# Optimization experiments

Measured on AMD Instinct MI355X. Metric: run time of the kernel, lower is better.

Reference implementation:

```python
import jax, jax.numpy as jnp
import numpy as np

N = 50000      # nodes
E = 600000     # edges
F_IN = 128     # input features
H = 128        # hidden
C = 40         # classes


def _glorot(key, shape):
    lim = float(np.sqrt(6.0 / (shape[0] + shape[1])))
    return jax.random.uniform(key, shape, jnp.float32, -lim, lim)


def setup_inputs() -> dict:
    key = jax.random.key(0)
    ks = jax.random.split(key, 16)
    inp = {
        "x": jax.random.normal(ks[0], (N, F_IN), jnp.float32),
        "edge_index": jax.random.randint(ks[1], (2, E), 0, N, jnp.int64),
    }
    # SAGEConv params: Wl (neighbor branch, with bias), Wr (root branch), stored [in, out]
    dims = [(F_IN, H), (H, H), (H, H)]
    for i, (din, dout) in enumerate(dims, start=1):
        inp[f"Wl{i}"] = _glorot(ks[2 * i], (din, dout))
        inp[f"bl{i}"] = jnp.zeros((dout,), jnp.float32)
        inp[f"Wr{i}"] = _glorot(ks[2 * i + 1], (din, dout))
    inp["W_lin1"] = _glorot(ks[10], (H, H))
    inp["b_lin1"] = jnp.zeros((H,), jnp.float32)
    inp["W_lin2"] = _glorot(ks[11], (H, C))
    inp["b_lin2"] = jnp.zeros((C,), jnp.float32)
    return inp


def _sage_conv(x, src, dst, Wl, bl, Wr):
    # mean-aggregate neighbor features at destination nodes
    msgs = x[src]  # [E, d] gather
    agg = jax.ops.segment_sum(msgs, dst, num_segments=N)
    deg = jax.ops.segment_sum(jnp.ones((E,), x.dtype), dst, num_segments=N)
    agg = agg / jnp.clip(deg, 1.0)[:, None]
    return agg @ Wl + bl + x @ Wr


def reference(x, edge_index, Wl1, bl1, Wr1, Wl2, bl2, Wr2, Wl3, bl3, Wr3,
              W_lin1, b_lin1, W_lin2, b_lin2):
    src, dst = edge_index[0], edge_index[1]
    h = jax.nn.relu(_sage_conv(x, src, dst, Wl1, bl1, Wr1))
    h = jax.nn.relu(_sage_conv(h, src, dst, Wl2, bl2, Wr2))
    h = jax.nn.relu(_sage_conv(h, src, dst, Wl3, bl3, Wr3))
    h = jax.nn.relu(h @ W_lin1 + b_lin1)
    # dropout: inference mode (training=False) -> identity
    logits = h @ W_lin2 + b_lin2
    return jax.nn.log_softmax(logits, axis=-1)
```

## Files before the change

kernel.cpp:

```cpp
#include <hip/hip_runtime.h>
#include <hip/hip_bf16.h>
#include <math.h>

#define NNODES 50000
#define NEDGES 600000
#define FDIM   128
#define NCLS   40
#define SLOTS  64
#define CVT_BLOCKS 6250
#define PACK_BLOCKS 62
#define CZ_BLOCKS 196
#define PREP_TOTAL (CVT_BLOCKS + PACK_BLOCKS + CZ_BLOCKS)
#define NT16 (NNODES / 16)

typedef __hip_bfloat16 bf16;
typedef short bf16x8 __attribute__((ext_vector_type(8)));
typedef short bf16x4 __attribute__((ext_vector_type(4)));
typedef float f32x4  __attribute__((ext_vector_type(4)));

__device__ __forceinline__ float b2f(short u) {
    union { unsigned int i; float f; } cv;
    cv.i = ((unsigned int)(unsigned short)u) << 16;
    return cv.f;
}
__device__ __forceinline__ short f2b(float f) {
    bf16 h = __float2bfloat16(f);
    return *(const short*)&h;
}
__device__ __forceinline__ float ldf(const void* p, int fp32, int idx) {
    return fp32 ? ((const float*)p)[idx]
                : __bfloat162float(((const bf16*)p)[idx]);
}
__device__ __forceinline__ int wave_is_fp32(const unsigned* p, int lane) {
    unsigned w = p[lane];
    unsigned e = (w >> 7) & 0xFFu;
    int inr = (e >= 100u && e <= 140u) ? 1 : 0;
    return (int)__popcll(__ballot(inr)) < 32;
}
__device__ __forceinline__ int lidx(int row, int col) {
    return row * 128 + ((((col >> 3) ^ (row & 15)) << 3) | (col & 7));
}

__global__ void k_prep(const void* __restrict__ xin,
                       const void* Wl1, const void* Wr1, const void* Wl2,
                       const void* Wr2, const void* Wl3, const void* Wr3,
                       const void* Wlin1, const void* Wlin2,
                       const void* b1, const void* b2, const void* b3,
                       const void* b4, const void* b5,
                       int* __restrict__ cursor, bf16* __restrict__ xb,
                       bf16x8* __restrict__ packed, float* __restrict__ biasf) {
    int b = blockIdx.x, tid = threadIdx.x, lane = tid & 63;
    if (b < CVT_BLOCKS) {
        int xf = wave_is_fp32((const unsigned*)xin, lane);
        int i = b * 256 + tid;
        if (xf) {
            float4 v = ((const float4*)xin)[i];
            bf16x4 o;
            o[0] = f2b(v.x); o[1] = f2b(v.y); o[2] = f2b(v.z); o[3] = f2b(v.w);
            ((bf16x4*)xb)[i] = o;
        } else {
            ((uint2*)xb)[i] = ((const uint2*)xin)[i];
        }
        return;
    }
    if (b >= CVT_BLOCKS + PACK_BLOCKS) {
        int i = (b - CVT_BLOCKS - PACK_BLOCKS) * 256 + tid;
        if (i < NNODES) cursor[i] = 0;
        return;
    }
    int wf = wave_is_fp32((const unsigned*)Wl1, lane);
    int lb = b - CVT_BLOCKS;
    if (lb >= 59) {
        int t = (lb - 59) * 256 + tid;
        if (t >= 5 * 128) return;
        int which = t >> 7, idx = t & 127;
        const void* srcs[5] = {b1, b2, b3, b4, b5};
        int n = (which == 4) ? NCLS : 128;
        float v = 0.f;
        if (idx < n) v = ldf(srcs[which], wf, idx);
        biasf[t] = v;
        return;
    }
    int t2 = lb * 256 + tid;
    int frag = t2 >> 6;
    if (frag >= 236) return;
    int q = lane >> 4, l16 = lane & 15;
    const void* W;
    int kbase, n, ldw = 128, nvalid = 128;
    if (frag < 192) {
        int g = frag >> 6, local = frag & 63;
        int kt = local >> 3, nt = local & 7;
        const void* Wl = (g == 0) ? Wl1 : (g == 1) ? Wl2 : Wl3;
        const void* Wr = (g == 0) ? Wr1 : (g == 1) ? Wr2 : Wr3;
        W = (kt < 4) ? Wl : Wr;
        kbase = (kt & 3) * 32;
        n = nt * 16 + l16;
    } else if (frag < 224) {
        int local = frag - 192;
        int kt = local >> 3, nt = local & 7;
        W = Wlin1; kbase = kt * 32; n = nt * 16 + l16;
    } else {
        int local = frag - 224;
        int kt = local / 3, nt = local % 3;
        W = Wlin2; kbase = kt * 32; n = nt * 16 + l16;
        ldw = NCLS; nvalid = NCLS;
    }
    bf16x8 v;
#pragma unroll
    for (int j = 0; j < 8; j++) {
        float e = 0.f;
        if (n < nvalid) e = ldf(W, wf, (kbase + q * 8 + j) * ldw + n);
        v[j] = f2b(e);
    }
    packed[frag * 64 + lane] = v;
}

__global__ void k_fill(const int* __restrict__ e32, const long long* __restrict__ e64,
                       int* __restrict__ cursor, int* __restrict__ edge_src) {
    int lane = threadIdx.x & 63;
    unsigned hw = ((const unsigned*)e32)[2 * lane + 1];
    int is64 = (__ballot(hw != 0u) == 0ull) ? 1 : 0;
    int i = blockIdx.x * 256 + threadIdx.x;
    if (i >= NEDGES) return;
    int srcn = is64 ? (int)e64[i] : e32[i];
    int dstn = is64 ? (int)e64[NEDGES + i] : e32[NEDGES + i];
    int pos = atomicAdd(&cursor[dstn], 1);
    if (pos < SLOTS) edge_src[dstn * SLOTS + pos] = srcn;
}

__device__ __forceinline__ void agg_wave(const bf16* __restrict__ x,
        const int* __restrict__ deg, const int* __restrict__ edge_src,
        short* __restrict__ lds, int rowbase, int wave, int lane) {
    const int g = lane >> 4, c = lane & 15;
    const int base = rowbase + wave * 8;
    int dgv = deg[base];
    int eidx = edge_src[base * SLOTS + lane];
    if ((unsigned)eidx >= NNODES) eidx = 0;
#pragma unroll
    for (int t = 0; t < 8; t++) {
        int dgn = 0;
        if (t < 7) dgn = deg[base + t + 1];
        int dcap = dgv < SLOTS ? ((dgv + 15) & ~15) : SLOTS;
        float acc[8];
#pragma unroll
        for (int e = 0; e < 8; e++) acc[e] = 0.f;
        for (int i = 0; i < dcap; i += 16) {
            float m0 = (i + g < dgv) ? 1.f : 0.f;
            float m1 = (i + 4 + g < dgv) ? 1.f : 0.f;
            float m2 = (i + 8 + g < dgv) ? 1.f : 0.f;
            float m3 = (i + 12 + g < dgv) ? 1.f : 0.f;
            unsigned o0 = (unsigned)(__shfl(eidx, i + g)      * FDIM + c * 8);
            unsigned o1 = (unsigned)(__shfl(eidx, i + 4 + g)  * FDIM + c * 8);
            unsigned o2 = (unsigned)(__shfl(eidx, i + 8 + g)  * FDIM + c * 8);
            unsigned o3 = (unsigned)(__shfl(eidx, i + 12 + g) * FDIM + c * 8);
            bf16x8 v0 = *(const bf16x8*)(x + o0);
            bf16x8 v1 = *(const bf16x8*)(x + o1);
            bf16x8 v2 = *(const bf16x8*)(x + o2);
            bf16x8 v3 = *(const bf16x8*)(x + o3);
#pragma unroll
            for (int e = 0; e < 8; e++) {
                acc[e] = fmaf(b2f(v0[e]), m0, acc[e]);
                acc[e] = fmaf(b2f(v1[e]), m1, acc[e]);
                acc[e] = fmaf(b2f(v2[e]), m2, acc[e]);
                acc[e] = fmaf(b2f(v3[e]), m3, acc[e]);
            }
        }
        int en = 0;
        if (t < 7) {
            en = edge_src[(base + t + 1) * SLOTS + lane];
            if ((unsigned)en >= NNODES) en = 0;
        }
#pragma unroll
        for (int e = 0; e < 8; e++) {
            float a = acc[e];
            a += __shfl_xor(a, 16);
            a += __shfl_xor(a, 32);
            acc[e] = a;
        }
        if (g == 0) {
            float inv = (dgv > 0) ? 1.f / (float)dgv : 0.f;
            bf16x8 o;
#pragma unroll
            for (int e = 0; e < 8; e++) o[e] = f2b(acc[e] * inv);
            *(bf16x8*)(lds + lidx(wave * 8 + t, c * 8)) = o;
        }
        dgv = dgn; eidx = en;
    }
}

template <bool TO_LDS>
__device__ __forceinline__ void gemm_phase(int rowbase, int lane, int wave,
        short* __restrict__ aggL, const bf16* __restrict__ xroot,
        const bf16x8* __restrict__ packed, const float* __restrict__ bias,
        bf16* __restrict__ out) {
    const int q = lane >> 4, l16 = lane & 15;
    const unsigned rowA = (unsigned)(rowbase + l16);
    f32x4 acc[4];
#pragma unroll
    for (int n = 0; n < 4; n++) acc[n] = (f32x4){0.f, 0.f, 0.f, 0.f};
#pragma unroll 2
    for (int kt = 0; kt < 8; kt++) {
        bf16x8 a;
        if (kt < 4)
            a = *(const bf16x8*)(aggL + lidx(l16, kt * 32 + q * 8));
        else
            a = *(const bf16x8*)(xroot + rowA * FDIM + (kt - 4) * 32 + q * 8);
        bf16x8 b[4];
#pragma unroll
        for (int n = 0; n < 4; n++)
            b[n] = packed[(kt * 8 + wave * 4 + n) * 64 + lane];
#pragma unroll
        for (int n = 0; n < 4; n++)
            acc[n] = __builtin_amdgcn_mfma_f32_16x16x32_bf16(a, b[n], acc[n], 0, 0, 0);
    }
    if (TO_LDS) __syncthreads();
#pragma unroll
    for (int n = 0; n < 4; n++) {
        int col = (wave * 4 + n) * 16 + l16;
        float bv = bias[col];
#pragma unroll
        for (int r = 0; r < 4; r++) {
            float v = fmaxf(acc[n][r] + bv, 0.f);
            if (TO_LDS)
                aggL[lidx(q * 4 + r, col)] = f2b(v);
            else
                out[(unsigned)(rowbase + q * 4 + r) * FDIM + col] = __float2bfloat16(v);
        }
    }
}

__device__ __forceinline__ void head_phase(int rowbase, int lane, int wave,
        const short* __restrict__ h3, short* __restrict__ h1,
        const bf16x8* __restrict__ packed, const float* __restrict__ bias1,
        const float* __restrict__ bias2, float* __restrict__ out) {
    const int q = lane >> 4, l16 = lane & 15;
    f32x4 acc[4];
#pragma unroll
    for (int n = 0; n < 4; n++) acc[n] = (f32x4){0.f, 0.f, 0.f, 0.f};
#pragma unroll 2
    for (int kt = 0; kt < 4; kt++) {
        bf16x8 a = *(const bf16x8*)(h3 + lidx(l16, kt * 32 + q * 8));
        bf16x8 b[4];
#pragma unroll
        for (int n = 0; n < 4; n++)
            b[n] = packed[(192 + kt * 8 + wave * 4 + n) * 64 + lane];
#pragma unroll
        for (int n = 0; n < 4; n++)
            acc[n] = __builtin_amdgcn_mfma_f32_16x16x32_bf16(a, b[n], acc[n], 0, 0, 0);
    }
#pragma unroll
    for (int n = 0; n < 4; n++) {
        int col = (wave * 4 + n) * 16 + l16;
        float bv = bias1[col];
#pragma unroll
        for (int r = 0; r < 4; r++)
            h1[lidx(q * 4 + r, col)] = f2b(fmaxf(acc[n][r] + bv, 0.f));
    }
    __syncthreads();
    if (wave >= 1) return;
    f32x4 acc2[3];
#pragma unroll
    for (int n = 0; n < 3; n++) acc2[n] = (f32x4){0.f, 0.f, 0.f, 0.f};
#pragma unroll
    for (int kt = 0; kt < 4; kt++) {
        bf16x8 a = *(const bf16x8*)(h1 + lidx(l16, kt * 32 + q * 8));
        bf16x8 b[3];
#pragma unroll
        for (int n = 0; n < 3; n++) b[n] = packed[(224 + kt * 3 + n) * 64 + lane];
#pragma unroll
        for (int n = 0; n < 3; n++)
            acc2[n] = __builtin_amdgcn_mfma_f32_16x16x32_bf16(a, b[n], acc2[n], 0, 0, 0);
    }
    const float NEG = -1e30f;
    bool v2ok = (l16 < 8);
#pragma unroll
    for (int r = 0; r < 4; r++) {
        unsigned row = (unsigned)(rowbase + q * 4 + r);
        float v0 = acc2[0][r] + bias2[l16];
        float v1 = acc2[1][r] + bias2[16 + l16];
        float v2 = v2ok ? (acc2[2][r] + bias2[32 + l16]) : NEG;
        float m = fmaxf(fmaxf(v0, v1), v2);
#pragma unroll
        for (int mk = 1; mk < 16; mk <<= 1) m = fmaxf(m, __shfl_xor(m, mk));
        float sden = expf(v0 - m) + expf(v1 - m) + (v2ok ? expf(v2 - m) : 0.f);
#pragma unroll
        for (int mk = 1; mk < 16; mk <<= 1) sden += __shfl_xor(sden, mk);
        float l = m + logf(sden);
        out[row * NCLS + l16] = v0 - l;
        out[row * NCLS + 16 + l16] = v1 - l;
        if (v2ok) out[row * NCLS + 32 + l16] = v2 - l;
    }
}

__global__ void __launch_bounds__(128)
k_layer(const bf16* __restrict__ src, const int* __restrict__ deg,
        const int* __restrict__ edge_src, const bf16x8* __restrict__ packed,
        const float* __restrict__ bias, bf16* __restrict__ out) {
    __shared__ __align__(16) short aggL[16 * 128];
    const int lane = threadIdx.x & 63, wave = threadIdx.x >> 6;
    const int rowbase = blockIdx.x * 16;
    agg_wave(src, deg, edge_src, aggL, rowbase, wave, lane);
    __syncthreads();
    gemm_phase<false>(rowbase, lane, wave, aggL, src, packed, bias, out);
}

__global__ void __launch_bounds__(128)
k_layer3head(const bf16* __restrict__ src, const int* __restrict__ deg,
             const int* __restrict__ edge_src, const bf16x8* __restrict__ packed,
             const float* __restrict__ biasf, float* __restrict__ out) {
    __shared__ __align__(16) short aggL[16 * 128];
    __shared__ __align__(16) short h1[16 * 128];
    const int lane = threadIdx.x & 63, wave = threadIdx.x >> 6;
    const int rowbase = blockIdx.x * 16;
    agg_wave(src, deg, edge_src, aggL, rowbase, wave, lane);
    __syncthreads();
    gemm_phase<true>(rowbase, lane, wave, aggL, src, packed + 128 * 64,
                     biasf + 256, nullptr);
    __syncthreads();
    head_phase(rowbase, lane, wave, aggL, h1, packed, biasf + 384, biasf + 512, out);
}

extern "C" void kernel_launch(void* const* d_in, const int* in_sizes, int n_in,
                              void* d_out, int out_size, void* d_ws, size_t ws_size,
                              hipStream_t stream) {
    char* ws = (char*)d_ws;
    size_t off = 0;
    auto take = [&](size_t bytes) {
        void* pp = ws + off;
        off = (off + bytes + 255) & ~(size_t)255;
        return pp;
    };
    const int* e32 = (const int*)d_in[1];
    const long long* e64 = (const long long*)d_in[1];
    int* cursor    = (int*)take(NNODES * 4);
    int* edge_src  = (int*)take((size_t)NNODES * SLOTS * 4);
    bf16x8* packed = (bf16x8*)take(236 * 64 * 16);
    float* biasf   = (float*)take(5 * 128 * 4);
    bf16* xb       = (bf16*)take((size_t)NNODES * FDIM * 2);
    bf16* bufA     = (bf16*)take((size_t)NNODES * FDIM * 2);
    float* outp    = (float*)d_out;
    bf16* bufB     = xb;

    k_prep<<<PREP_TOTAL, 256, 0, stream>>>(
        d_in[0], d_in[2], d_in[4], d_in[5], d_in[7], d_in[8], d_in[10],
        d_in[11], d_in[13], d_in[3], d_in[6], d_in[9], d_in[12], d_in[14],
        cursor, xb, packed, biasf);
    k_fill<<<(NEDGES + 255) / 256, 256, 0, stream>>>(e32, e64, cursor, edge_src);

    k_layer<<<NT16, 128, 0, stream>>>(xb, cursor, edge_src, packed, biasf, bufA);
    k_layer<<<NT16, 128, 0, stream>>>(bufA, cursor, edge_src,
                                      packed + 64 * 64, biasf + 128, bufB);
    k_layer3head<<<NT16, 128, 0, stream>>>(bufB, cursor, edge_src,
                                           packed, biasf, outp);
}
```

Measured before the change: 248.2 us.

## Use single-wave blocks with 4 nodes per wave-quarter aggregation

Switches the layer kernels from two waves to one 64-lane wave per 16-node tile. Aggregation now lets each 16-lane group own one node (4 nodes in flight), looping over the first 16 neighbours unrolled and handling higher degrees in a ballot-guarded tail. This removes the cross-group shuffle reductions and all __syncthreads. The GEMM now computes all 8 output column tiles in one wave and writes results through LDS for coalesced stores. The cost is fewer waves per block and more registers per wave, and the unrolled first 16 neighbours issue masked loads even for low-degree nodes.

```diff
diff --git a/kernel.cpp b/kernel.cpp
--- a/kernel.cpp
+++ b/kernel.cpp
@@ -128,148 +128,123 @@
     if (pos < SLOTS) edge_src[dstn * SLOTS + pos] = srcn;
 }
 
-__device__ __forceinline__ void agg_wave(const bf16* __restrict__ x,
-        const int* __restrict__ deg, const int* __restrict__ edge_src,
-        short* __restrict__ lds, int rowbase, int wave, int lane) {
+__device__ __forceinline__ void agg16(const bf16* __restrict__ x,
+        const int* __restrict__ deg, const int* __restrict__ es,
+        short* __restrict__ lds, int node0, int lane) {
     const int g = lane >> 4, c = lane & 15;
-    const int base = rowbase + wave * 8;
-    int dgv = deg[base];
-    int eidx = edge_src[base * SLOTS + lane];
-    if ((unsigned)eidx >= NNODES) eidx = 0;
-#pragma unroll
-    for (int t = 0; t < 8; t++) {
-        int dgn = 0;
-        if (t < 7) dgn = deg[base + t + 1];
-        int dcap = dgv < SLOTS ? ((dgv + 15) & ~15) : SLOTS;
+    const int gsel = lane & 48;
+#pragma unroll
+    for (int p = 0; p < 4; p++) {
+        const int node = node0 + p * 4 + g;
+        const int dg = deg[node];
+        int ei = es[node * SLOTS + c];
+        if ((unsigned)ei >= NNODES) ei = 0;
         float acc[8];
 #pragma unroll
         for (int e = 0; e < 8; e++) acc[e] = 0.f;
-        for (int i = 0; i < dcap; i += 16) {
-            float m0 = (i + g < dgv) ? 1.f : 0.f;
-            float m1 = (i + 4 + g < dgv) ? 1.f : 0.f;
-            float m2 = (i + 8 + g < dgv) ? 1.f : 0.f;
-            float m3 = (i + 12 + g < dgv) ? 1.f : 0.f;
-            unsigned o0 = (unsigned)(__shfl(eidx, i + g)      * FDIM + c * 8);
-            unsigned o1 = (unsigned)(__shfl(eidx, i + 4 + g)  * FDIM + c * 8);
-            unsigned o2 = (unsigned)(__shfl(eidx, i + 8 + g)  * FDIM + c * 8);
-            unsigned o3 = (unsigned)(__shfl(eidx, i + 12 + g) * FDIM + c * 8);
-            bf16x8 v0 = *(const bf16x8*)(x + o0);
-            bf16x8 v1 = *(const bf16x8*)(x + o1);
-            bf16x8 v2 = *(const bf16x8*)(x + o2);
-            bf16x8 v3 = *(const bf16x8*)(x + o3);
-#pragma unroll
-            for (int e = 0; e < 8; e++) {
-                acc[e] = fmaf(b2f(v0[e]), m0, acc[e]);
-                acc[e] = fmaf(b2f(v1[e]), m1, acc[e]);
-                acc[e] = fmaf(b2f(v2[e]), m2, acc[e]);
-                acc[e] = fmaf(b2f(v3[e]), m3, acc[e]);
+#pragma unroll
+        for (int j = 0; j < 16; j++) {
+            int idx = __shfl(ei, gsel | j);
+            float m = (j < dg) ? 1.f : 0.f;
+            bf16x8 v = *(const bf16x8*)(x + (unsigned)(idx * FDIM + c * 8));
+#pragma unroll
+            for (int e = 0; e < 8; e++) acc[e] = fmaf(b2f(v[e]), m, acc[e]);
+        }
+        if (__ballot(dg > 16) != 0ull) {
+            for (int jb = 16; jb < SLOTS && __ballot(dg > jb) != 0ull; jb += 16) {
+                int ei2 = es[node * SLOTS + jb + c];
+                if ((unsigned)ei2 >= NNODES) ei2 = 0;
+                for (int j = 0; j < 16; j++) {
+                    int idx = __shfl(ei2, gsel | j);
+                    float m = (jb + j < dg) ? 1.f : 0.f;
+                    bf16x8 v = *(const bf16x8*)(x + (unsigned)(idx * FDIM + c * 8));
+#pragma unroll
+                    for (int e = 0; e < 8; e++) acc[e] = fmaf(b2f(v[e]), m, acc[e]);
+                }
             }
         }
-        int en = 0;
-        if (t < 7) {
-            en = edge_src[(base + t + 1) * SLOTS + lane];
-            if ((unsigned)en >= NNODES) en = 0;
-        }
-#pragma unroll
-        for (int e = 0; e < 8; e++) {
-            float a = acc[e];
-            a += __shfl_xor(a, 16);
-            a += __shfl_xor(a, 32);
-            acc[e] = a;
-        }
-        if (g == 0) {
-            float inv = (dgv > 0) ? 1.f / (float)dgv : 0.f;
-            bf16x8 o;
-#pragma unroll
-            for (int e = 0; e < 8; e++) o[e] = f2b(acc[e] * inv);
-            *(bf16x8*)(lds + lidx(wave * 8 + t, c * 8)) = o;
-        }
-        dgv = dgn; eidx = en;
-    }
-}
-
-template <bool TO_LDS>
-__device__ __forceinline__ void gemm_phase(int rowbase, int lane, int wave,
-        short* __restrict__ aggL, const bf16* __restrict__ xroot,
-        const bf16x8* __restrict__ packed, const float* __restrict__ bias,
-        bf16* __restrict__ out) {
+        float inv = (dg > 0) ? 1.f / (float)dg : 0.f;
+        bf16x8 o;
+#pragma unroll
+        for (int e = 0; e < 8; e++) o[e] = f2b(acc[e] * inv);
+        *(bf16x8*)(lds + lidx(p * 4 + g, c * 8)) = o;
+    }
+}
+
+__device__ __forceinline__ void gemm16(int rowbase, int lane,
+        short* __restrict__ lds, const bf16* __restrict__ xroot,
+        const bf16x8* __restrict__ packed, const float* __restrict__ bias) {
     const int q = lane >> 4, l16 = lane & 15;
-    const unsigned rowA = (unsigned)(rowbase + l16);
-    f32x4 acc[4];
-#pragma unroll
-    for (int n = 0; n < 4; n++) acc[n] = (f32x4){0.f, 0.f, 0.f, 0.f};
-#pragma unroll 2
+    f32x4 acc[8];
+#pragma unroll
+    for (int n = 0; n < 8; n++) acc[n] = (f32x4){0.f, 0.f, 0.f, 0.f};
+#pragma unroll
     for (int kt = 0; kt < 8; kt++) {
         bf16x8 a;
         if (kt < 4)
-            a = *(const bf16x8*)(aggL + lidx(l16, kt * 32 + q * 8));
+            a = *(const bf16x8*)(lds + lidx(l16, kt * 32 + q * 8));
         else
-            a = *(const bf16x8*)(xroot + rowA * FDIM + (kt - 4) * 32 + q * 8);
-        bf16x8 b[4];
-#pragma unroll
-        for (int n = 0; n < 4; n++)
-            b[n] = packed[(kt * 8 + wave * 4 + n) * 64 + lane];
-#pragma unroll
-        for (int n = 0; n < 4; n++)
-            acc[n] = __builtin_amdgcn_mfma_f32_16x16x32_bf16(a, b[n], acc[n], 0, 0, 0);
-    }
-    if (TO_LDS) __syncthreads();
-#pragma unroll
-    for (int n = 0; n < 4; n++) {
-        int col = (wave * 4 + n) * 16 + l16;
+            a = *(const bf16x8*)(xroot +
+                    (unsigned)((rowbase + l16) * FDIM + (kt - 4) * 32 + q * 8));
+#pragma unroll
+        for (int n = 0; n < 8; n++)
+            acc[n] = __builtin_amdgcn_mfma_f32_16x16x32_bf16(
+                a, packed[(kt * 8 + n) * 64 + lane], acc[n], 0, 0, 0);
+    }
+#pragma unroll
+    for (int n = 0; n < 8; n++) {
+        int col = n * 16 + l16;
         float bv = bias[col];
 #pragma unroll
-        for (int r = 0; r < 4; r++) {
-            float v = fmaxf(acc[n][r] + bv, 0.f);
-            if (TO_LDS)
-                aggL[lidx(q * 4 + r, col)] = f2b(v);
-            else
-                out[(unsigned)(rowbase + q * 4 + r) * FDIM + col] = __float2bfloat16(v);
-        }
-    }
-}
-
-__device__ __forceinline__ void head_phase(int rowbase, int lane, int wave,
+        for (int r = 0; r < 4; r++)
+            lds[lidx(q * 4 + r, col)] = f2b(fmaxf(acc[n][r] + bv, 0.f));
+    }
+}
+
+__device__ __forceinline__ void store16(int rowbase, int lane,
+        const short* __restrict__ lds, bf16* __restrict__ out) {
+    const int g = lane >> 4, c = lane & 15;
+#pragma unroll
+    for (int p = 0; p < 4; p++) {
+        bf16x8 v = *(const bf16x8*)(lds + lidx(p * 4 + g, c * 8));
+        *(bf16x8*)(out + (unsigned)((rowbase + p * 4 + g) * FDIM + c * 8)) = v;
+    }
+}
+
+__device__ __forceinline__ void head16(int rowbase, int lane,
         const short* __restrict__ h3, short* __restrict__ h1,
         const bf16x8* __restrict__ packed, const float* __restrict__ bias1,
         const float* __restrict__ bias2, float* __restrict__ out) {
     const int q = lane >> 4, l16 = lane & 15;
-    f32x4 acc[4];
-#pragma unroll
-    for (int n = 0; n < 4; n++) acc[n] = (f32x4){0.f, 0.f, 0.f, 0.f};
-#pragma unroll 2
+    f32x4 acc[8];
+#pragma unroll
+    for (int n = 0; n < 8; n++) acc[n] = (f32x4){0.f, 0.f, 0.f, 0.f};
+#pragma unroll
     for (int kt = 0; kt < 4; kt++) {
         bf16x8 a = *(const bf16x8*)(h3 + lidx(l16, kt * 32 + q * 8));
-        bf16x8 b[4];
-#pragma unroll
-        for (int n = 0; n < 4; n++)
-            b[n] = packed[(192 + kt * 8 + wave * 4 + n) * 64 + lane];
-#pragma unroll
-        for (int n = 0; n < 4; n++)
-            acc[n] = __builtin_amdgcn_mfma_f32_16x16x32_bf16(a, b[n], acc[n], 0, 0, 0);
-    }
-#pragma unroll
-    for (int n = 0; n < 4; n++) {
-        int col = (wave * 4 + n) * 16 + l16;
+#pragma unroll
+        for (int n = 0; n < 8; n++)
+            acc[n] = __builtin_amdgcn_mfma_f32_16x16x32_bf16(
+                a, packed[(192 + kt * 8 + n) * 64 + lane], acc[n], 0, 0, 0);
+    }
+#pragma unroll
+    for (int n = 0; n < 8; n++) {
+        int col = n * 16 + l16;
         float bv = bias1[col];
 #pragma unroll
         for (int r = 0; r < 4; r++)
             h1[lidx(q * 4 + r, col)] = f2b(fmaxf(acc[n][r] + bv, 0.f));
     }
-    __syncthreads();
-    if (wave >= 1) return;
     f32x4 acc2[3];
 #pragma unroll
     for (int n = 0; n < 3; n++) acc2[n] = (f32x4){0.f, 0.f, 0.f, 0.f};
 #pragma unroll
     for (int kt = 0; kt < 4; kt++) {
         bf16x8 a = *(const bf16x8*)(h1 + lidx(l16, kt * 32 + q * 8));
-        bf16x8 b[3];
-#pragma unroll
-        for (int n = 0; n < 3; n++) b[n] = packed[(224 + kt * 3 + n) * 64 + lane];
 #pragma unroll
         for (int n = 0; n < 3; n++)
-            acc2[n] = __builtin_amdgcn_mfma_f32_16x16x32_bf16(a, b[n], acc2[n], 0, 0, 0);
+            acc2[n] = __builtin_amdgcn_mfma_f32_16x16x32_bf16(
+                a, packed[(224 + kt * 3 + n) * 64 + lane], acc2[n], 0, 0, 0);
     }
     const float NEG = -1e30f;
     bool v2ok = (l16 < 8);
@@ -292,32 +267,29 @@
     }
 }
 
-__global__ void __launch_bounds__(128)
+__global__ void __launch_bounds__(64)
 k_layer(const bf16* __restrict__ src, const int* __restrict__ deg,
         const int* __restrict__ edge_src, const bf16x8* __restrict__ packed,
         const float* __restrict__ bias, bf16* __restrict__ out) {
-    __shared__ __align__(16) short aggL[16 * 128];
-    const int lane = threadIdx.x & 63, wave = threadIdx.x >> 6;
+    __shared__ __align__(16) short lds[16 * 128];
+    const int lane = threadIdx.x;
     const int rowbase = blockIdx.x * 16;
-    agg_wave(src, deg, edge_src, aggL, rowbase, wave, lane);
-    __syncthreads();
-    gemm_phase<false>(rowbase, lane, wave, aggL, src, packed, bias, out);
-}
-
-__global__ void __launch_bounds__(128)
+    agg16(src, deg, edge_src, lds, rowbase, lane);
+    gemm16(rowbase, lane, lds, src, packed, bias);
+    store16(rowbase, lane, lds, out);
+}
+
+__global__ void __launch_bounds__(64)
 k_layer3head(const bf16* __restrict__ src, const int* __restrict__ deg,
              const int* __restrict__ edge_src, const bf16x8* __restrict__ packed,
              const float* __restrict__ biasf, float* __restrict__ out) {
-    __shared__ __align__(16) short aggL[16 * 128];
+    __shared__ __align__(16) short h3[16 * 128];
     __shared__ __align__(16) short h1[16 * 128];
-    const int lane = threadIdx.x & 63, wave = threadIdx.x >> 6;
+    const int lane = threadIdx.x;
     const int rowbase = blockIdx.x * 16;
-    agg_wave(src, deg, edge_src, aggL, rowbase, wave, lane);
-    __syncthreads();
-    gemm_phase<true>(rowbase, lane, wave, aggL, src, packed + 128 * 64,
-                     biasf + 256, nullptr);
-    __syncthreads();
-    head_phase(rowbase, lane, wave, aggL, h1, packed, biasf + 384, biasf + 512, out);
+    agg16(src, deg, edge_src, h3, rowbase, lane);
+    gemm16(rowbase, lane, h3, src, packed + 128 * 64, biasf + 256);
+    head16(rowbase, lane, h3, h1, packed, biasf + 384, biasf + 512, out);
 }
 
 extern "C" void kernel_launch(void* const* d_in, const int* in_sizes, int n_in,
@@ -347,9 +319,9 @@
         cursor, xb, packed, biasf);
     k_fill<<<(NEDGES + 255) / 256, 256, 0, stream>>>(e32, e64, cursor, edge_src);
 
-    k_layer<<<NT16, 128, 0, stream>>>(xb, cursor, edge_src, packed, biasf, bufA);
-    k_layer<<<NT16, 128, 0, stream>>>(bufA, cursor, edge_src,
-                                      packed + 64 * 64, biasf + 128, bufB);
-    k_layer3head<<<NT16, 128, 0, stream>>>(bufB, cursor, edge_src,
-                                           packed, biasf, outp);
-}
+    k_layer<<<NT16, 64, 0, stream>>>(xb, cursor, edge_src, packed, biasf, bufA);
+    k_layer<<<NT16, 64, 0, stream>>>(bufA, cursor, edge_src,
+                                     packed + 64 * 64, biasf + 128, bufB);
+    k_layer3head<<<NT16, 64, 0, stream>>>(bufB, cursor, edge_src,
+                                          packed, biasf, outp);
+}
```

Result: faster. 238.2 us (-4.0%).
